# Kernel optimization log

Measured on AMD Instinct MI355X. Metric: run time of the kernel, lower is better.

The kernel has to match this reference:

```python
import jax, jax.numpy as jnp
import numpy as np

B, C, H, W = 128, 1280, 16, 16


def _conv1x1(x, w, b):
    # 1x1 conv == per-pixel linear over channels: (O,C) x (B,C,H,W) -> (B,O,H,W)
    return jnp.einsum('oc,bchw->bohw', w, x) + b[None, :, None, None]


def setup_inputs() -> dict:
    key = jax.random.key(0)
    ks = jax.random.split(key, 10)
    s = 1.0 / np.sqrt(C)
    inp = {
        'x': jax.random.normal(ks[0], (B, C, H, W), dtype=jnp.float32),
        'Wk': jax.random.uniform(ks[1], (C, C), jnp.float32, -s, s),
        'bk': jax.random.uniform(ks[2], (C,), jnp.float32, -s, s),
        'Wq': jax.random.uniform(ks[3], (C, C), jnp.float32, -s, s),
        'bq': jax.random.uniform(ks[4], (C,), jnp.float32, -s, s),
        'Wv': jax.random.uniform(ks[5], (C, C), jnp.float32, -s, s),
        'bv': jax.random.uniform(ks[6], (C,), jnp.float32, -s, s),
        'Wr': jax.random.uniform(ks[7], (C, C), jnp.float32, -s, s),
        'br': jax.random.uniform(ks[8], (C,), jnp.float32, -s, s),
        'alpha': 0.1 * jax.random.normal(ks[9], (1,), dtype=jnp.float32),
    }
    return inp


def reference(x, Wk, bk, Wq, bq, Wv, bv, Wr, br, alpha):
    b, c, h, w = x.shape
    hw = h * w
    k = _conv1x1(x, Wk, bk).reshape(b, c, hw)   # (B,C,HW)
    q = _conv1x1(x, Wq, bq).reshape(b, c, hw)   # (B,C,HW)
    v = _conv1x1(x, Wv, bv).reshape(b, c, hw)   # (B,C,HW)
    # K^T Q: (B,HW,HW) == keys.view.permute(0,2,1) @ queries.view
    scores = jnp.einsum('bcn,bcm->bnm', k, q)
    # torch.nn.Softmax2d on a 3D tensor applies softmax over dim=-3 (here: batch)
    attn = jax.nn.softmax(scores, axis=0)
    # attn @ V^T: (B,HW,HW) @ (B,HW,C) -> (B,HW,C)
    att = jnp.einsum('bnm,bmc->bnc', attn, v.transpose(0, 2, 1))
    att = att.transpose(0, 2, 1).reshape(b, c, h, w)
    out = _conv1x1(att, Wr, br)
    return alpha * out + x
```

## Files before the change

### kernel.cpp

```cpp
#include <hip/hip_runtime.h>
#include <hip/hip_bf16.h>

typedef __attribute__((ext_vector_type(8))) short bf16x8;
typedef __attribute__((ext_vector_type(4))) float f32x4;

#define GLD16(g, s) __builtin_amdgcn_global_load_lds( \
    (const __attribute__((address_space(1))) void*)(g), \
    (__attribute__((address_space(3))) void*)(s), 16, 0, 0)

#define SBAR() __builtin_amdgcn_sched_barrier(0)
#define WAIT_LGKM(n) do { asm volatile("s_waitcnt lgkmcnt(" #n ")" ::: "memory"); SBAR(); } while (0)

static constexpr int kB  = 128;
static constexpr int kC  = 1280;
static constexpr int kHW = 256;

__device__ __forceinline__ float bf2f(unsigned short u) {
    return __uint_as_float(((unsigned int)u) << 16);
}

template<int OUT_MODE, int BIAS_MODE, int ORDER>
__device__ __forceinline__ void gemm_body(
    const __hip_bfloat16* __restrict__ A,
    const __hip_bfloat16* __restrict__ Bt,
    void* __restrict__ outp,
    const float* __restrict__ bias,
    const float* __restrict__ resid,
    const float* __restrict__ alphap,
    const float* __restrict__ aux1,
    const float* __restrict__ aux2,
    int M, int N, int K,
    int ldA, int ldB, long sA, long sB, long sC, int ldC,
    char* smem, int z)
{
    const int t = threadIdx.x;
    const int w = t >> 6, l = t & 63;
    const int q = l >> 4, r16 = l & 15;
    const int wr = w >> 2, wc = w & 3;
    const int nbm = M >> 8, nbn = N >> 8;
    const int nwg = nbm * nbn;
    int f = blockIdx.x;
    {
        const int q8 = nwg >> 3, r8 = nwg & 7;
        const int xcd = f & 7, rank = f >> 3;
        f = (xcd < r8 ? xcd * (q8 + 1) : r8 * (q8 + 1) + (xcd - r8) * q8) + rank;
    }
    long m0, n0;
    if (ORDER == 0) { m0 = (long)(f % nbm) << 8; n0 = (long)(f / nbm) << 8; }
    else            { n0 = (long)(f % nbn) << 8; m0 = (long)(f / nbn) << 8; }
    const char* Azb = (const char*)(A + (long)z * sA);
    const char* Bzb = (const char*)(Bt + (long)z * sB);

    const char* pa[4];
    const char* pb[4];
    int ldsd[4];
    #pragma unroll
    for (int i = 0; i < 4; ++i) {
        const int d = i * 8192 + t * 16;
        const int row = d >> 7;
        const int cb = (d & 127) ^ ((row & 7) << 4);
        pa[i] = Azb + ((m0 + row) * (long)ldA) * 2 + cb;
        pb[i] = Bzb + ((n0 + row) * (long)ldB) * 2 + cb;
        ldsd[i] = d;
    }
    auto stage = [&](int slot) {
        char* base = smem + slot * 65536;
        #pragma unroll
        for (int i = 0; i < 4; ++i) GLD16(pa[i], base + ldsd[i]);
        #pragma unroll
        for (int i = 0; i < 4; ++i) GLD16(pb[i], base + 32768 + ldsd[i]);
        #pragma unroll
        for (int i = 0; i < 4; ++i) { pa[i] += 128; pb[i] += 128; }
    };

    const int mask = (l & 7) << 4;
    const int cx  = (q << 4) ^ mask;
    int offA[2], offB[2];
    offA[0] = (wr * 128 + r16) * 128 + cx;
    offA[1] = (wr * 128 + r16) * 128 + (cx ^ 64);
    offB[0] = 32768 + (wc * 64 + r16) * 128 + cx;
    offB[1] = 32768 + (wc * 64 + r16) * 128 + (cx ^ 64);

#define DSA(dst, bs_, mih, kk) do { const char* p_ = (bs_) + offA[kk] + (mih) * 8192; \
    dst[0] = *(const bf16x8*)(p_);        dst[1] = *(const bf16x8*)(p_ + 2048); \
    dst[2] = *(const bf16x8*)(p_ + 4096); dst[3] = *(const bf16x8*)(p_ + 6144); } while (0)
#define DSB(dst, bs_, kk) do { const char* p_ = (bs_) + offB[kk]; \
    dst[0] = *(const bf16x8*)(p_);        dst[1] = *(const bf16x8*)(p_ + 2048); \
    dst[2] = *(const bf16x8*)(p_ + 4096); dst[3] = *(const bf16x8*)(p_ + 6144); } while (0)
#define MM16(ar, br, mih) do { __builtin_amdgcn_s_setprio(1); \
    _Pragma("unroll") for (int j = 0; j < 4; ++j) \
    _Pragma("unroll") for (int ni = 0; ni < 4; ++ni) \
        acc[(mih) * 4 + j][ni] = __builtin_amdgcn_mfma_f32_16x16x32_bf16( \
            ar[j], br[ni], acc[(mih) * 4 + j][ni], 0, 0, 0); \
    __builtin_amdgcn_s_setprio(0); SBAR(); } while (0)

    f32x4 acc[8][4] = {};
    const int nK = K >> 6;
    stage(0);

    for (int tk = 0; tk < nK; ++tk) {
        const int s = tk & 1;
        asm volatile("s_waitcnt vmcnt(0)" ::: "memory");
        SBAR();
        __builtin_amdgcn_s_barrier();
        SBAR();
        if (tk + 1 < nK) stage(s ^ 1);
        SBAR();

        const char* bs_ = smem + s * 65536;
        bf16x8 aP[4], bP[4], aQ[4], bQ[4];
        DSB(bP, bs_, 0); DSA(aP, bs_, 0, 0);
        DSA(aQ, bs_, 1, 0);
        WAIT_LGKM(4);  MM16(aP, bP, 0);
        DSB(bQ, bs_, 1); DSA(aP, bs_, 0, 1);
        WAIT_LGKM(8);  MM16(aQ, bP, 1);
        DSA(aQ, bs_, 1, 1);
        WAIT_LGKM(4);  MM16(aP, bQ, 0);
        WAIT_LGKM(0);  MM16(aQ, bQ, 1);
        asm volatile("s_waitcnt lgkmcnt(0)" ::: "memory");
        SBAR();
        __builtin_amdgcn_s_barrier();
        SBAR();
    }

    const float alpha = (OUT_MODE >= 3) ? alphap[0] : 0.0f;
    #pragma unroll
    for (int mi = 0; mi < 8; ++mi) {
        #pragma unroll
        for (int ni = 0; ni < 4; ++ni) {
            #pragma unroll
            for (int r = 0; r < 4; ++r) {
                const long row = m0 + wr * 128 + mi * 16 + q * 4 + r;
                const long col = n0 + wc * 64 + ni * 16 + r16;
                float vv = acc[mi][ni][r];
                if (BIAS_MODE == 1) vv += bias[col];
                if (BIAS_MODE == 2) vv += bias[row];
                if (OUT_MODE == 0) {
                    ((__hip_bfloat16*)outp)[(long)z * sC + row * ldC + col] = __float2bfloat16(vv);
                } else if (OUT_MODE == 1) {
                    ((float*)outp)[(long)z * sC + row * ldC + col] = vv;
                } else if (OUT_MODE == 2) {
                    const long addr = (col >> 8) * (long)(kC * kHW) + row * kHW + (col & 255);
                    ((__hip_bfloat16*)outp)[addr] = __float2bfloat16(vv);
                } else if (OUT_MODE == 3) {
                    const long addr = (col >> 8) * (long)(kC * kHW) + row * kHW + (col & 255);
                    ((float*)outp)[addr] = alpha * vv + resid[addr];
                } else {
                    const long addr = (long)z * (kC * kHW) + row * kHW + col;
                    const float term = vv + aux1[row] * aux2[(long)z * 256 + col] + bias[row];
                    ((float*)outp)[addr] = alpha * term + resid[addr];
                }
            }
        }
    }
#undef DSA
#undef DSB
#undef MM16
}

template<int OUT_MODE, int BIAS_MODE, int ORDER>
__global__ __launch_bounds__(512, 2) void gemm_q(
    const __hip_bfloat16* __restrict__ A,
    const __hip_bfloat16* __restrict__ Bt,
    void* __restrict__ outp,
    const float* __restrict__ bias,
    const float* __restrict__ resid,
    const float* __restrict__ alphap,
    const float* __restrict__ aux1,
    const float* __restrict__ aux2,
    int M, int N, int K,
    int ldA, int ldB, long sA, long sB, long sC, int ldC)
{
    extern __shared__ char smem[];
    gemm_body<OUT_MODE, BIAS_MODE, ORDER>(A, Bt, outp, bias, resid, alphap,
        aux1, aux2, M, N, K, ldA, ldB, sA, sB, sC, ldC, smem, blockIdx.z);
}

__global__ __launch_bounds__(512, 2) void gemm_dual(
    const __hip_bfloat16* __restrict__ xT,
    const __hip_bfloat16* __restrict__ G,
    __hip_bfloat16* __restrict__ uT,
    const float* __restrict__ w1,
    const __hip_bfloat16* __restrict__ W2,
    __hip_bfloat16* __restrict__ rv)
{
    extern __shared__ char smem[];
    if (blockIdx.z == 0) {
        gemm_body<0, 1, 1>(xT, G, uT, w1, nullptr, nullptr, nullptr, nullptr,
            32768, 1280, 1280, 1280, 1280, 0, 0, 0, 1280, smem, 0);
    } else {
        gemm_body<2, 0, 0>(W2, xT, rv, nullptr, nullptr, nullptr, nullptr, nullptr,
            1280, 32768, 1280, 1280, 1280, 0, 0, 0, 0, smem, 0);
    }
}

__global__ __launch_bounds__(512, 2) void gemm_gsplit(
    const __hip_bfloat16* __restrict__ WkT,
    const __hip_bfloat16* __restrict__ WqT,
    const __hip_bfloat16* __restrict__ Wrb,
    const __hip_bfloat16* __restrict__ WvT,
    float* __restrict__ Gp)
{
    extern __shared__ char smem[];
    const int zz = blockIdx.z;
    const int pair = zz >> 1, ks = zz & 1;
    const __hip_bfloat16* A  = (pair ? Wrb : WkT) + ks * 640;
    const __hip_bfloat16* Bt = (pair ? WvT : WqT) + ks * 640;
    gemm_body<1, 0, 0>(A, Bt, Gp, nullptr, nullptr, nullptr, nullptr, nullptr,
        1280, 1280, 640, 1280, 1280, 0, 0, 1638400, 1280, smem, zz);
}

__global__ __launch_bounds__(256) void reduce_gw(
    const float* __restrict__ Gp,
    __hip_bfloat16* __restrict__ G, __hip_bfloat16* __restrict__ W2)
{
    const long i = ((long)blockIdx.x * 256 + threadIdx.x) * 4;
    const float4 a = *reinterpret_cast<const float4*>(Gp + i);
    const float4 b = *reinterpret_cast<const float4*>(Gp + 1638400 + i);
    G[i + 0] = __float2bfloat16(a.x + b.x);
    G[i + 1] = __float2bfloat16(a.y + b.y);
    G[i + 2] = __float2bfloat16(a.z + b.z);
    G[i + 3] = __float2bfloat16(a.w + b.w);
    const float4 c = *reinterpret_cast<const float4*>(Gp + 2L * 1638400 + i);
    const float4 d = *reinterpret_cast<const float4*>(Gp + 3L * 1638400 + i);
    W2[i + 0] = __float2bfloat16(c.x + d.x);
    W2[i + 1] = __float2bfloat16(c.y + d.y);
    W2[i + 2] = __float2bfloat16(c.z + d.z);
    W2[i + 3] = __float2bfloat16(c.w + d.w);
}

__global__ __launch_bounds__(512, 2) void gemm_scores(
    const __hip_bfloat16* __restrict__ xT,
    const __hip_bfloat16* __restrict__ uT,
    float* __restrict__ sc)
{
    extern __shared__ char smem[];
    const int b = blockIdx.z >> 1, kh = blockIdx.z & 1;
    const __hip_bfloat16* A  = xT + (long)b * 327680 + kh * 640;
    const __hip_bfloat16* Bt = uT + (long)b * 327680 + kh * 640;
    float* out = sc + (long)kh * 8388608;
    gemm_body<1, 0, 0>(A, Bt, out, nullptr, nullptr, nullptr, nullptr, nullptr,
        256, 256, 640, 1280, 1280, 0, 0, 65536, 256, smem, b);
}

__global__ __launch_bounds__(256) void transpose_x(
    const float* __restrict__ x, __hip_bfloat16* __restrict__ xT,
    const float* __restrict__ w2, float* __restrict__ c2s)
{
    __shared__ float tile[64][65];
    __shared__ float red[4][64];
    const int b = blockIdx.z;
    const int c0 = blockIdx.x * 64;
    const int p0 = blockIdx.y * 64;
    const int tj = threadIdx.x & 63;
    const int ti = threadIdx.x >> 6;
    const float* xb = x + ((long)b * kC + c0) * kHW + p0;
    #pragma unroll
    for (int i = 0; i < 16; ++i) {
        const int c = i * 4 + ti;
        tile[c][tj] = xb[(long)c * kHW + tj];
    }
    __syncthreads();
    __hip_bfloat16* o = xT + ((long)(b * kHW + p0)) * kC + c0;
    #pragma unroll
    for (int i = 0; i < 16; ++i) {
        const int p = i * 4 + ti;
        o[(long)p * kC + tj] = __float2bfloat16(tile[tj][p]);
    }
    float s = 0.0f;
    #pragma unroll
    for (int j = 0; j < 16; ++j)
        s += tile[ti * 16 + j][tj] * w2[c0 + ti * 16 + j];
    red[ti][tj] = s;
    __syncthreads();
    if (ti == 0)
        atomicAdd(&c2s[b * 256 + p0 + tj], red[0][tj] + red[1][tj] + red[2][tj] + red[3][tj]);
}

__global__ __launch_bounds__(256) void transpose_w4(
    const float* __restrict__ Wk, __hip_bfloat16* __restrict__ WkT,
    const float* __restrict__ Wq, __hip_bfloat16* __restrict__ WqT,
    const float* __restrict__ Wv, __hip_bfloat16* __restrict__ WvT,
    const float* __restrict__ Wr, __hip_bfloat16* __restrict__ Wrb)
{
    const int zz = blockIdx.z;
    const float* W = (zz == 0) ? Wk : (zz == 1) ? Wq : (zz == 2) ? Wv : Wr;
    __hip_bfloat16* WT = (zz == 0) ? WkT : (zz == 1) ? WqT : (zz == 2) ? WvT : Wrb;
    __shared__ float tile[64][65];
    const int o0 = blockIdx.x * 64;
    const int c0 = blockIdx.y * 64;
    const int tj = threadIdx.x & 63;
    const int ti = threadIdx.x >> 6;
    #pragma unroll
    for (int i = 0; i < 16; ++i) {
        const int o = i * 4 + ti;
        tile[o][tj] = W[(long)(o0 + o) * kC + c0 + tj];
    }
    __syncthreads();
    if (zz < 3) {
        #pragma unroll
        for (int i = 0; i < 16; ++i) {
            const int c = i * 4 + ti;
            WT[(long)(c0 + c) * kC + o0 + tj] = __float2bfloat16(tile[tj][c]);
        }
    } else {
        #pragma unroll
        for (int i = 0; i < 16; ++i) {
            const int o = i * 4 + ti;
            WT[(long)(o0 + o) * kC + c0 + tj] = __float2bfloat16(tile[o][tj]);
        }
    }
}

__global__ __launch_bounds__(256) void zero_f32(float* __restrict__ p)
{
    reinterpret_cast<float4*>(p)[blockIdx.x * 256 + threadIdx.x] =
        make_float4(0.f, 0.f, 0.f, 0.f);
}

__global__ __launch_bounds__(256) void preproc_small(
    const float* __restrict__ Wk, const float* __restrict__ bq,
    const float* __restrict__ Wq, const float* __restrict__ bk,
    const float* __restrict__ Wr, const float* __restrict__ bv,
    float* __restrict__ w1, float* __restrict__ w2,
    float* __restrict__ wrbv, float* __restrict__ c0out)
{
    const int bidx = blockIdx.x;
    if (bidx < 40) {
        const int y = bidx / 20;
        const int bx = bidx % 20;
        const float* W = y ? Wq : Wk;
        const float* v = y ? bk : bq;
        float* out = y ? w2 : w1;
        const int lj = threadIdx.x & 63;
        const int wid = threadIdx.x >> 6;
        const int c = bx * 64 + lj;
        __shared__ float red[4][64];
        float s = 0.0f;
        for (int o = wid * 320; o < (wid + 1) * 320; ++o)
            s += W[(long)o * kC + c] * v[o];
        red[wid][lj] = s;
        __syncthreads();
        if (wid == 0) out[c] = red[0][lj] + red[1][lj] + red[2][lj] + red[3][lj];
    } else if (bidx < 360) {
        const int bx = bidx - 40;
        const int wid = threadIdx.x >> 6, lj = threadIdx.x & 63;
        const int o = bx * 4 + wid;
        float s = 0.0f;
        #pragma unroll
        for (int j = 0; j < 20; ++j)
            s += Wr[(long)o * kC + j * 64 + lj] * bv[j * 64 + lj];
        #pragma unroll
        for (int off = 32; off > 0; off >>= 1) s += __shfl_down(s, off);
        if (lj == 0) wrbv[o] = s;
    } else {
        __shared__ float red[256];
        const int t_ = threadIdx.x;
        float s = 0.0f;
        for (int j = t_; j < kC; j += 256) s += bk[j] * bq[j];
        red[t_] = s; __syncthreads();
        for (int off = 128; off > 0; off >>= 1) {
            if (t_ < off) red[t_] += red[t_ + off];
            __syncthreads();
        }
        if (t_ == 0) c0out[0] = red[0];
    }
}

__global__ __launch_bounds__(256) void rowsum_attn(
    const __hip_bfloat16* __restrict__ attn, float* __restrict__ rs)
{
    const int wid = threadIdx.x >> 6, lj = threadIdx.x & 63;
    const long p = (long)blockIdx.x * 4 + wid;
    const ushort4 v = *(const ushort4*)((const char*)attn + p * 512 + lj * 8);
    float s = bf2f(v.x) + bf2f(v.y) + bf2f(v.z) + bf2f(v.w);
    #pragma unroll
    for (int off = 32; off > 0; off >>= 1) s += __shfl_down(s, off);
    if (lj == 0) rs[p] = s;
}

__global__ __launch_bounds__(256) void softmax_batch(
    const float* __restrict__ sc, __hip_bfloat16* __restrict__ attn,
    const float* __restrict__ c2s, const float* __restrict__ c0p)
{
    const int pos = blockIdx.x * 256 + threadIdx.x;
    const int mcol = pos & 255;
    const float c0v = c0p[0];
    const float* sc1 = sc + 8388608;
    float m = -3.0e38f, s = 0.0f;
    for (int b = 0; b < kB; ++b) {
        const long i = (long)b * 65536 + pos;
        const float v = sc[i] + sc1[i] + c2s[b * 256 + mcol] + c0v;
        const float mn = fmaxf(m, v);
        s = s * __expf(m - mn) + __expf(v - mn);
        m = mn;
    }
    const float rinv = 1.0f / s;
    for (int b = 0; b < kB; ++b) {
        const long i = (long)b * 65536 + pos;
        const float v = sc[i] + sc1[i] + c2s[b * 256 + mcol] + c0v;
        attn[i] = __float2bfloat16(__expf(v - m) * rinv);
    }
}

extern "C" void kernel_launch(void* const* d_in, const int* in_sizes, int n_in,
                              void* d_out, int out_size, void* d_ws, size_t ws_size,
                              hipStream_t stream)
{
    const float* x  = (const float*)d_in[0];
    const float* Wk = (const float*)d_in[1];
    const float* bk = (const float*)d_in[2];
    const float* Wq = (const float*)d_in[3];
    const float* bq = (const float*)d_in[4];
    const float* Wv = (const float*)d_in[5];
    const float* bv = (const float*)d_in[6];
    const float* Wr = (const float*)d_in[7];
    const float* br = (const float*)d_in[8];
    const float* al = (const float*)d_in[9];

    char* ws = (char*)d_ws;
    __hip_bfloat16* xT   = (__hip_bfloat16*)(ws);
    __hip_bfloat16* uT   = (__hip_bfloat16*)(ws + 83886080L);
    __hip_bfloat16* attn = (__hip_bfloat16*)(ws + 83886080L);
    __hip_bfloat16* rv   = (__hip_bfloat16*)(ws + 167772160L);
    float*          Gp   = (float*)(ws + 167772160L);
    float*          sc   = (float*)(ws + 251658240L);
    __hip_bfloat16* WkT  = (__hip_bfloat16*)(ws + 318767104L);
    __hip_bfloat16* Wrb  = (__hip_bfloat16*)(ws + 322043904L);
    __hip_bfloat16* WqT  = (__hip_bfloat16*)(ws + 325320704L);
    __hip_bfloat16* WvT  = (__hip_bfloat16*)(ws + 328597504L);
    __hip_bfloat16* G    = (__hip_bfloat16*)(ws + 331874304L);
    __hip_bfloat16* W2   = (__hip_bfloat16*)(ws + 335151104L);
    float*          w1   = (float*)(ws + 338427904L);
    float*          w2v  = (float*)(ws + 338433024L);
    float*          wrbv = (float*)(ws + 338438144L);
    float*          c0b  = (float*)(ws + 338443264L);
    float*          c2s  = (float*)(ws + 338443776L);
    float*          rs   = (float*)(ws + 338574848L);

    const int SMEM = 131072;
    hipFuncSetAttribute((const void*)gemm_q<4,0,0>, hipFuncAttributeMaxDynamicSharedMemorySize, SMEM);
    hipFuncSetAttribute((const void*)gemm_dual,   hipFuncAttributeMaxDynamicSharedMemorySize, SMEM);
    hipFuncSetAttribute((const void*)gemm_gsplit, hipFuncAttributeMaxDynamicSharedMemorySize, SMEM);
    hipFuncSetAttribute((const void*)gemm_scores, hipFuncAttributeMaxDynamicSharedMemorySize, SMEM);

    transpose_w4<<<dim3(20, 20, 4), 256, 0, stream>>>(Wk, WkT, Wq, WqT, Wv, WvT, Wr, Wrb);
    preproc_small<<<361, 256, 0, stream>>>(Wk, bq, Wq, bk, Wr, bv, w1, w2v, wrbv, c0b);
    zero_f32<<<32, 256, 0, stream>>>(c2s);
    transpose_x<<<dim3(20, 4, 128), 256, 0, stream>>>(x, xT, w2v, c2s);

    gemm_gsplit<<<dim3(25, 1, 4), 512, SMEM, stream>>>(WkT, WqT, Wrb, WvT, Gp);
    reduce_gw<<<1600, 256, 0, stream>>>(Gp, G, W2);
    gemm_dual<<<dim3(640, 1, 2), 512, SMEM, stream>>>(xT, G, uT, w1, W2, rv);
    gemm_scores<<<dim3(1, 1, 256), 512, SMEM, stream>>>(xT, uT, sc);
    softmax_batch<<<256, 256, 0, stream>>>(sc, attn, c2s, c0b);
    rowsum_attn<<<8192, 256, 0, stream>>>(attn, rs);
    gemm_q<4, 0, 0><<<dim3(5, 1, 128), 512, SMEM, stream>>>(rv, attn, d_out,
        br, x, al, wrbv, rs,
        1280, 256, 256, 256, 256, 327680, 65536, 0, 0);
}
```

Baseline: 491.4 us.

## Switch GEMM mainloop to 4-slot K=32 ring buffer with three stages in flight

The K tile is halved from 64 to 32 and the two-slot LDS double buffer becomes a four-slot ring that keeps three global-to-LDS stages in flight. Waits use partial vmcnt counts, and the trailing per-iteration barrier is dropped. The XOR swizzle goes away because the 64-byte row layout already gives contiguous LDS reads. The aim is to hide more global-load latency with one barrier per iteration, at the cost of twice as many iterations and less MFMA work per barrier.

```diff
diff --git a/kernel.cpp b/kernel.cpp
--- a/kernel.cpp
+++ b/kernel.cpp
@@ -51,42 +51,36 @@
     const char* Azb = (const char*)(A + (long)z * sA);
     const char* Bzb = (const char*)(Bt + (long)z * sB);
 
-    const char* pa[4];
-    const char* pb[4];
-    int ldsd[4];
-    #pragma unroll
-    for (int i = 0; i < 4; ++i) {
+    const char* pa[2];
+    const char* pb[2];
+    int ldsd[2];
+    #pragma unroll
+    for (int i = 0; i < 2; ++i) {
         const int d = i * 8192 + t * 16;
-        const int row = d >> 7;
-        const int cb = (d & 127) ^ ((row & 7) << 4);
-        pa[i] = Azb + ((m0 + row) * (long)ldA) * 2 + cb;
-        pb[i] = Bzb + ((n0 + row) * (long)ldB) * 2 + cb;
+        const int row = d >> 6;
+        const int col = d & 63;
+        pa[i] = Azb + ((m0 + row) * (long)ldA) * 2 + col;
+        pb[i] = Bzb + ((n0 + row) * (long)ldB) * 2 + col;
         ldsd[i] = d;
     }
     auto stage = [&](int slot) {
-        char* base = smem + slot * 65536;
-        #pragma unroll
-        for (int i = 0; i < 4; ++i) GLD16(pa[i], base + ldsd[i]);
-        #pragma unroll
-        for (int i = 0; i < 4; ++i) GLD16(pb[i], base + 32768 + ldsd[i]);
-        #pragma unroll
-        for (int i = 0; i < 4; ++i) { pa[i] += 128; pb[i] += 128; }
+        char* base = smem + slot * 32768;
+        GLD16(pa[0], base + ldsd[0]);
+        GLD16(pa[1], base + ldsd[1]);
+        GLD16(pb[0], base + 16384 + ldsd[0]);
+        GLD16(pb[1], base + 16384 + ldsd[1]);
+        pa[0] += 64; pa[1] += 64; pb[0] += 64; pb[1] += 64;
     };
 
-    const int mask = (l & 7) << 4;
-    const int cx  = (q << 4) ^ mask;
-    int offA[2], offB[2];
-    offA[0] = (wr * 128 + r16) * 128 + cx;
-    offA[1] = (wr * 128 + r16) * 128 + (cx ^ 64);
-    offB[0] = 32768 + (wc * 64 + r16) * 128 + cx;
-    offB[1] = 32768 + (wc * 64 + r16) * 128 + (cx ^ 64);
-
-#define DSA(dst, bs_, mih, kk) do { const char* p_ = (bs_) + offA[kk] + (mih) * 8192; \
-    dst[0] = *(const bf16x8*)(p_);        dst[1] = *(const bf16x8*)(p_ + 2048); \
-    dst[2] = *(const bf16x8*)(p_ + 4096); dst[3] = *(const bf16x8*)(p_ + 6144); } while (0)
-#define DSB(dst, bs_, kk) do { const char* p_ = (bs_) + offB[kk]; \
-    dst[0] = *(const bf16x8*)(p_);        dst[1] = *(const bf16x8*)(p_ + 2048); \
-    dst[2] = *(const bf16x8*)(p_ + 4096); dst[3] = *(const bf16x8*)(p_ + 6144); } while (0)
+    const int aoff = (wr * 128 + r16) * 64 + q * 16;
+    const int boff = 16384 + (wc * 64 + r16) * 64 + q * 16;
+
+#define DSA(dst, bs_, mih) do { const char* p_ = (bs_) + aoff + (mih) * 4096; \
+    dst[0] = *(const bf16x8*)(p_);        dst[1] = *(const bf16x8*)(p_ + 1024); \
+    dst[2] = *(const bf16x8*)(p_ + 2048); dst[3] = *(const bf16x8*)(p_ + 3072); } while (0)
+#define DSB(dst, bs_) do { const char* p_ = (bs_) + boff; \
+    dst[0] = *(const bf16x8*)(p_);        dst[1] = *(const bf16x8*)(p_ + 1024); \
+    dst[2] = *(const bf16x8*)(p_ + 2048); dst[3] = *(const bf16x8*)(p_ + 3072); } while (0)
 #define MM16(ar, br, mih) do { __builtin_amdgcn_s_setprio(1); \
     _Pragma("unroll") for (int j = 0; j < 4; ++j) \
     _Pragma("unroll") for (int ni = 0; ni < 4; ++ni) \
@@ -95,32 +89,32 @@
     __builtin_amdgcn_s_setprio(0); SBAR(); } while (0)
 
     f32x4 acc[8][4] = {};
-    const int nK = K >> 6;
+    const int nK = K >> 5;
+
     stage(0);
+    if (nK > 1) stage(1);
+    if (nK > 2) stage(2);
 
     for (int tk = 0; tk < nK; ++tk) {
-        const int s = tk & 1;
-        asm volatile("s_waitcnt vmcnt(0)" ::: "memory");
+        const int rem = nK - 1 - tk;
+        if (rem >= 2)      { asm volatile("s_waitcnt vmcnt(8)" ::: "memory"); }
+        else if (rem == 1) { asm volatile("s_waitcnt vmcnt(4)" ::: "memory"); }
+        else               { asm volatile("s_waitcnt vmcnt(0)" ::: "memory"); }
         SBAR();
         __builtin_amdgcn_s_barrier();
         SBAR();
-        if (tk + 1 < nK) stage(s ^ 1);
+
+        const char* bs_ = smem + (tk & 3) * 32768;
+        bf16x8 a0[4], a1[4], b0[4];
+        DSB(b0, bs_);
+        DSA(a0, bs_, 0);
+        DSA(a1, bs_, 1);
+        if (tk + 3 < nK) stage((tk + 3) & 3);
         SBAR();
-
-        const char* bs_ = smem + s * 65536;
-        bf16x8 aP[4], bP[4], aQ[4], bQ[4];
-        DSB(bP, bs_, 0); DSA(aP, bs_, 0, 0);
-        DSA(aQ, bs_, 1, 0);
-        WAIT_LGKM(4);  MM16(aP, bP, 0);
-        DSB(bQ, bs_, 1); DSA(aP, bs_, 0, 1);
-        WAIT_LGKM(8);  MM16(aQ, bP, 1);
-        DSA(aQ, bs_, 1, 1);
-        WAIT_LGKM(4);  MM16(aP, bQ, 0);
-        WAIT_LGKM(0);  MM16(aQ, bQ, 1);
-        asm volatile("s_waitcnt lgkmcnt(0)" ::: "memory");
-        SBAR();
-        __builtin_amdgcn_s_barrier();
-        SBAR();
+        WAIT_LGKM(4);
+        MM16(a0, b0, 0);
+        WAIT_LGKM(0);
+        MM16(a1, b0, 1);
     }
 
     const float alpha = (OUT_MODE >= 3) ? alphap[0] : 0.0f;
```

Measured after the change: 517.3 us. 5.3% more time.
